# Kernel optimization log

Measured on AMD Instinct MI355X. Metric: run time of the kernel, lower is better.

The kernel has to match this reference:

```python
import jax, jax.numpy as jnp
import numpy as np

N, NS, C_IN, C_OUT = 20000, 32, 64, 128
V = (0.1, 0.1, 0.2)
BN_EPS = 1e-5


def setup_inputs() -> dict:
    key = jax.random.key(0)
    ks = jax.random.split(key, 5)
    features = jax.random.normal(ks[0], (N, NS, C_IN), jnp.float32)
    coords = jax.random.normal(ks[1], (N, NS, 3), jnp.float32)
    centers = jax.random.normal(ks[2], (N, 4), jnp.float32)
    mask = jax.random.randint(ks[3], (N, NS), 0, 2, jnp.int32)
    # Linear(C_IN, C_OUT, bias=False) weight, torch layout [out, in]
    W = jax.random.normal(ks[4], (C_OUT, C_IN), jnp.float32) / np.sqrt(C_IN)
    gamma = jnp.ones((C_OUT,), jnp.float32)   # BatchNorm1d weight
    beta = jnp.zeros((C_OUT,), jnp.float32)   # BatchNorm1d bias
    return dict(features=features, coords=coords, centers=centers, mask=mask,
                W=W, gamma=gamma, beta=beta)


def reference(features, coords, centers, mask, W, gamma, beta):
    # --- geometric features (no_grad in original) ---
    normalizer = jnp.array([V[0], V[1], V[2], V[0]**2 + V[1]**2 + V[2]**2],
                           dtype=jnp.float32)
    rel = coords - centers[:, 1:4][:, None, :]            # [N, NS, 3]
    dist = jnp.sum(rel * rel, axis=2, keepdims=True)       # [N, NS, 1]
    geo = jnp.concatenate([rel, dist], axis=2) / normalizer  # [N, NS, 4]

    # --- shared MLP: Linear -> BatchNorm1d (training stats) -> ReLU ---
    x = jnp.einsum('nsc,dc->nsd', features, W)             # [N, NS, C_OUT]
    xf = x.reshape(-1, C_OUT)
    mu = jnp.mean(xf, axis=0)
    var = jnp.mean((xf - mu) ** 2, axis=0)                 # biased var (torch BN)
    x = (x - mu) * jax.lax.rsqrt(var + BN_EPS) * gamma + beta
    x = jax.nn.relu(x)                                     # [N, NS, C_OUT]

    # --- weighted, masked mean pool over neighbors ---
    geo_rep = jnp.tile(geo, (1, 1, C_OUT // 4))            # [N, NS, C_OUT]
    m = mask.astype(jnp.float32)                           # [N, NS]
    num = jnp.sum(x * geo_rep * m[:, :, None], axis=1)     # [N, C_OUT]
    den = jnp.maximum(jnp.sum(m, axis=1, keepdims=True), 1.0)
    return num / den
```

## Files before the change

### kernel.cpp

```cpp
#include <hip/hip_runtime.h>
#include <hip/hip_bf16.h>

#define N_PTS 20000
#define NSAMP 32
#define CIN 64
#define COUT 128
#define M_ROWS (N_PTS * NSAMP)
#define TILES (M_ROWS / 64)
#define K1_BLOCKS 1024
#define K1_WAVES (K1_BLOCKS * 4)
#define BN_EPS 1e-5f

typedef __attribute__((ext_vector_type(8))) short short8v;
typedef __attribute__((ext_vector_type(4))) float f32x4;

__device__ inline short bf16_of(float f) {
    unsigned u = __float_as_uint(f);
    u = (u + 0x7FFFu + ((u >> 16) & 1u)) >> 16;
    return (short)u;
}

__global__ __launch_bounds__(256) void k1_stats(const float* __restrict__ F,
                                                float* __restrict__ Sp,
                                                float* __restrict__ Cp) {
    const int tid = threadIdx.x;
    const int wid = tid >> 6;
    const int lane = tid & 63;
    const int g = lane >> 4;
    const int i = lane & 15;
    const int gw = blockIdx.x * 4 + wid;

    f32x4 acc[4][4];
#pragma unroll
    for (int a = 0; a < 4; ++a)
#pragma unroll
        for (int b = 0; b < 4; ++b)
            acc[a][b] = (f32x4){0.f, 0.f, 0.f, 0.f};
    float colp[4] = {0.f, 0.f, 0.f, 0.f};

    for (int tile = gw; tile < TILES; tile += K1_WAVES) {
        const float* fb0 = F + (size_t)tile * 4096 + g * 512 + i;
        const float* fb1 = fb0 + 2048;
        short8v frag[4][2];
#pragma unroll
        for (int jt = 0; jt < 4; ++jt) {
            float cs = 0.f;
#pragma unroll
            for (int kk = 0; kk < 2; ++kk) {
                const float* p = kk ? fb1 : fb0;
                short8v fr;
#pragma unroll
                for (int r = 0; r < 8; ++r) {
                    float v = p[r * 64 + jt * 16];
                    cs += v;
                    fr[r] = bf16_of(v);
                }
                frag[jt][kk] = fr;
            }
            colp[jt] += cs;
        }
#pragma unroll
        for (int it = 0; it < 4; ++it)
#pragma unroll
            for (int jt = 0; jt < 4; ++jt) {
                acc[it][jt] = __builtin_amdgcn_mfma_f32_16x16x32_bf16(
                    frag[it][0], frag[jt][0], acc[it][jt], 0, 0, 0);
                acc[it][jt] = __builtin_amdgcn_mfma_f32_16x16x32_bf16(
                    frag[it][1], frag[jt][1], acc[it][jt], 0, 0, 0);
            }
    }

#pragma unroll
    for (int jt = 0; jt < 4; ++jt) {
        colp[jt] += __shfl_xor(colp[jt], 16);
        colp[jt] += __shfl_xor(colp[jt], 32);
    }
    if (lane < 16) {
#pragma unroll
        for (int jt = 0; jt < 4; ++jt)
            Cp[gw * 64 + jt * 16 + lane] = colp[jt];
    }

    __shared__ float sS[4096];
    for (int w = 0; w < 4; ++w) {
        if (wid == w) {
#pragma unroll
            for (int it = 0; it < 4; ++it)
#pragma unroll
                for (int jt = 0; jt < 4; ++jt)
#pragma unroll
                    for (int r = 0; r < 4; ++r) {
                        int idx = (it * 16 + g * 4 + r) * 64 + jt * 16 + i;
                        if (w == 0) sS[idx] = acc[it][jt][r];
                        else        sS[idx] += acc[it][jt][r];
                    }
        }
        __syncthreads();
    }
    float4* dst = (float4*)(Sp + (size_t)blockIdx.x * 4096);
    const float4* src = (const float4*)sS;
#pragma unroll
    for (int q = 0; q < 4; ++q)
        dst[q * 256 + tid] = src[q * 256 + tid];
}

__global__ __launch_bounds__(256) void kRedA(const float* __restrict__ Sp,
                                             const float* __restrict__ Cp,
                                             float* __restrict__ Tp,
                                             float* __restrict__ Tcp) {
    int t = blockIdx.x * 256 + threadIdx.x;
    if (t < 65536) {
        int o = t & 4095;
        int c = t >> 12;
        float s = 0.f;
#pragma unroll 8
        for (int b = 0; b < 64; ++b)
            s += Sp[(size_t)(c * 64 + b) * 4096 + o];
        Tp[t] = s;
    } else if (t < 65536 + 4096) {
        int u = t - 65536;
        int col = u & 63;
        int c = u >> 6;
        float s = 0.f;
#pragma unroll 8
        for (int w = 0; w < 64; ++w)
            s += Cp[(c * 64 + w) * 64 + col];
        Tcp[u] = s;
    }
}

__global__ __launch_bounds__(256) void kB(const float* __restrict__ Tp,
                                          const float* __restrict__ Tcp,
                                          const float* __restrict__ W,
                                          const float* __restrict__ gamma,
                                          const float* __restrict__ beta,
                                          float* __restrict__ scale,
                                          float* __restrict__ shift) {
    const int d = blockIdx.x;
    const int tid = threadIdx.x;
    __shared__ float sS[64 * 65];
    __shared__ float sw[64];

    for (int o = tid; o < 4096; o += 256) {
        float s = 0.f;
#pragma unroll
        for (int c = 0; c < 16; ++c) s += Tp[c * 4096 + o];
        sS[(o >> 6) * 65 + (o & 63)] = s;
    }
    if (tid < 64) sw[tid] = W[d * 64 + tid];
    __syncthreads();

    if (tid < 64) {
        float w_t = sw[tid];
        float rowdot = 0.f;
#pragma unroll
        for (int j = 0; j < 64; ++j) rowdot += sS[tid * 65 + j] * sw[j];
        float cs = 0.f;
#pragma unroll
        for (int c = 0; c < 64; ++c) cs += Tcp[c * 64 + tid];
        float p = w_t * rowdot;
        float mup = w_t * cs;
        for (int k = 1; k <= 32; k <<= 1) {
            p += __shfl_xor(p, k);
            mup += __shfl_xor(mup, k);
        }
        if (tid == 0) {
            const float invM = 1.f / (float)M_ROWS;
            float mu = mup * invM;
            float ex2 = p * invM;
            float var = ex2 - mu * mu;
            float rs = rsqrtf(var + BN_EPS);
            float sc = gamma[d] * rs;
            scale[d] = sc;
            shift[d] = beta[d] - mu * sc;
        }
    }
}

__global__ __launch_bounds__(256) void k2_main(const float* __restrict__ F,
                                               const float* __restrict__ coords,
                                               const float* __restrict__ centers,
                                               const int* __restrict__ mask,
                                               const float* __restrict__ W,
                                               const float* __restrict__ scale,
                                               const float* __restrict__ shift,
                                               float* __restrict__ out) {
    const int tid = threadIdx.x;
    const int wid = tid >> 6;
    const int lane = tid & 63;
    const int g = lane >> 4;
    const int i = lane & 15;
    const int n_base = (blockIdx.x * 4 + wid) * 4;

    float4 raw[8];
#define LOADA(nn)                                                            \
    do {                                                                     \
        const float* fb_ = F + ((size_t)(nn)*NSAMP) * 64;                    \
        _Pragma("unroll") for (int mt_ = 0; mt_ < 2; ++mt_)                  \
            _Pragma("unroll") for (int kk_ = 0; kk_ < 2; ++kk_) {            \
            const float* fp_ = fb_ + (mt_ * 16 + i) * 64 + kk_ * 32 + g * 8; \
            raw[mt_ * 4 + kk_ * 2 + 0] = *(const float4*)(fp_);              \
            raw[mt_ * 4 + kk_ * 2 + 1] = *(const float4*)(fp_ + 4);          \
        }                                                                    \
    } while (0)

    LOADA(n_base);

    short8v b[8][2];
#pragma unroll
    for (int t = 0; t < 8; ++t)
#pragma unroll
        for (int kk = 0; kk < 2; ++kk) {
            const float* wp = W + (t * 16 + i) * 64 + kk * 32 + g * 8;
            short8v fr;
#pragma unroll
            for (int r = 0; r < 8; ++r) fr[r] = bf16_of(wp[r]);
            b[t][kk] = fr;
        }
    float sc[8], sh[8];
#pragma unroll
    for (int t = 0; t < 8; ++t) {
        sc[t] = scale[t * 16 + i];
        sh[t] = shift[t * 16 + i];
    }

    __shared__ float geoM[4][32][4];
    const f32x4 Z = {0.f, 0.f, 0.f, 0.f};

    for (int it = 0; it < 4; ++it) {
        const int n = n_base + it;

        short8v a[2][2];
#pragma unroll
        for (int mt = 0; mt < 2; ++mt)
#pragma unroll
            for (int kk = 0; kk < 2; ++kk) {
                float4 lo = raw[mt * 4 + kk * 2 + 0];
                float4 hi = raw[mt * 4 + kk * 2 + 1];
                short8v fr;
                fr[0] = bf16_of(lo.x); fr[1] = bf16_of(lo.y);
                fr[2] = bf16_of(lo.z); fr[3] = bf16_of(lo.w);
                fr[4] = bf16_of(hi.x); fr[5] = bf16_of(hi.y);
                fr[6] = bf16_of(hi.z); fr[7] = bf16_of(hi.w);
                a[mt][kk] = fr;
            }

        if (it < 3) LOADA(n + 1);

        float m = 0.f;
        if (lane < 32) {
            const int s = lane;
            const float* cp = coords + ((size_t)n * NSAMP + s) * 3;
            float r0 = cp[0] - centers[n * 4 + 1];
            float r1 = cp[1] - centers[n * 4 + 2];
            float r2 = cp[2] - centers[n * 4 + 3];
            float dist = r0 * r0 + r1 * r1 + r2 * r2;
            m = (float)mask[n * NSAMP + s];
            float4 gm = make_float4(r0 * 10.f * m, r1 * 10.f * m,
                                    r2 * 5.f * m, dist * (1.f / 0.06f) * m);
            *(float4*)&geoM[wid][s][0] = gm;
        }
        float den = m;
        for (int k = 1; k <= 32; k <<= 1) den += __shfl_xor(den, k);
        float inv_den = 1.f / fmaxf(den, 1.f);

        __builtin_amdgcn_sched_barrier(0x7F);

        float gv[2][4];
        const int j0 = i & 3;
#pragma unroll
        for (int mt = 0; mt < 2; ++mt)
#pragma unroll
            for (int r = 0; r < 4; ++r)
                gv[mt][r] = geoM[wid][mt * 16 + g * 4 + r][j0];

#pragma unroll
        for (int t = 0; t < 8; ++t) {
            float nump = 0.f;
#pragma unroll
            for (int mt = 0; mt < 2; ++mt) {
                f32x4 acc = __builtin_amdgcn_mfma_f32_16x16x32_bf16(
                    a[mt][0], b[t][0], Z, 0, 0, 0);
                acc = __builtin_amdgcn_mfma_f32_16x16x32_bf16(
                    a[mt][1], b[t][1], acc, 0, 0, 0);
#pragma unroll
                for (int r = 0; r < 4; ++r) {
                    float v = fmaf(acc[r], sc[t], sh[t]);
                    v = fmaxf(v, 0.f);
                    nump = fmaf(v, gv[mt][r], nump);
                }
            }
            nump += __shfl_xor(nump, 16);
            nump += __shfl_xor(nump, 32);
            if (lane < 16)
                out[(size_t)n * COUT + t * 16 + lane] = nump * inv_den;
        }
    }
#undef LOADA
}

extern "C" void kernel_launch(void* const* d_in, const int* in_sizes, int n_in,
                              void* d_out, int out_size, void* d_ws, size_t ws_size,
                              hipStream_t stream) {
    const float* F = (const float*)d_in[0];
    const float* coords = (const float*)d_in[1];
    const float* centers = (const float*)d_in[2];
    const int* mask = (const int*)d_in[3];
    const float* W = (const float*)d_in[4];
    const float* gamma = (const float*)d_in[5];
    const float* beta = (const float*)d_in[6];
    float* out = (float*)d_out;

    float* wsf = (float*)d_ws;
    float* scale = wsf;
    float* shift = wsf + 128;
    float* Tp = wsf + 256;
    float* Tcp = Tp + 65536;
    float* Sp = Tcp + 4096;
    float* Cp = Sp + (size_t)K1_BLOCKS * 4096;

    k1_stats<<<K1_BLOCKS, 256, 0, stream>>>(F, Sp, Cp);
    kRedA<<<272, 256, 0, stream>>>(Sp, Cp, Tp, Tcp);
    kB<<<COUT, 256, 0, stream>>>(Tp, Tcp, W, gamma, beta, scale, shift);
    k2_main<<<1250, 256, 0, stream>>>(F, coords, centers, mask, W, scale, shift, out);
}
```

Measured before the change: 105.0 us.

## Use 1250 stats blocks with matching reduction chunks; drop manual prefetch in main kernel

```diff
diff --git a/kernel.cpp b/kernel.cpp
--- a/kernel.cpp
+++ b/kernel.cpp
@@ -7,8 +7,12 @@
 #define COUT 128
 #define M_ROWS (N_PTS * NSAMP)
 #define TILES (M_ROWS / 64)
-#define K1_BLOCKS 1024
+#define K1_BLOCKS 1250
 #define K1_WAVES (K1_BLOCKS * 4)
+#define SP_CHUNKS 25
+#define SP_DEPTH 50
+#define CP_CHUNKS 50
+#define CP_DEPTH 100
 #define BN_EPS 1e-5f
 
 typedef __attribute__((ext_vector_type(8))) short short8v;
@@ -109,22 +113,22 @@
                                              float* __restrict__ Tp,
                                              float* __restrict__ Tcp) {
     int t = blockIdx.x * 256 + threadIdx.x;
-    if (t < 65536) {
+    if (t < SP_CHUNKS * 4096) {
         int o = t & 4095;
         int c = t >> 12;
         float s = 0.f;
-#pragma unroll 8
-        for (int b = 0; b < 64; ++b)
-            s += Sp[(size_t)(c * 64 + b) * 4096 + o];
+#pragma unroll 10
+        for (int b = 0; b < SP_DEPTH; ++b)
+            s += Sp[(size_t)(c * SP_DEPTH + b) * 4096 + o];
         Tp[t] = s;
-    } else if (t < 65536 + 4096) {
-        int u = t - 65536;
+    } else if (t < SP_CHUNKS * 4096 + CP_CHUNKS * 64) {
+        int u = t - SP_CHUNKS * 4096;
         int col = u & 63;
         int c = u >> 6;
         float s = 0.f;
-#pragma unroll 8
-        for (int w = 0; w < 64; ++w)
-            s += Cp[(c * 64 + w) * 64 + col];
+#pragma unroll 10
+        for (int w = 0; w < CP_DEPTH; ++w)
+            s += Cp[(c * CP_DEPTH + w) * 64 + col];
         Tcp[u] = s;
     }
 }
@@ -144,7 +148,7 @@
     for (int o = tid; o < 4096; o += 256) {
         float s = 0.f;
 #pragma unroll
-        for (int c = 0; c < 16; ++c) s += Tp[c * 4096 + o];
+        for (int c = 0; c < SP_CHUNKS; ++c) s += Tp[c * 4096 + o];
         sS[(o >> 6) * 65 + (o & 63)] = s;
     }
     if (tid < 64) sw[tid] = W[d * 64 + tid];
@@ -157,7 +161,7 @@
         for (int j = 0; j < 64; ++j) rowdot += sS[tid * 65 + j] * sw[j];
         float cs = 0.f;
 #pragma unroll
-        for (int c = 0; c < 64; ++c) cs += Tcp[c * 64 + tid];
+        for (int c = 0; c < CP_CHUNKS; ++c) cs += Tcp[c * 64 + tid];
         float p = w_t * rowdot;
         float mup = w_t * cs;
         for (int k = 1; k <= 32; k <<= 1) {
@@ -192,20 +196,6 @@
     const int i = lane & 15;
     const int n_base = (blockIdx.x * 4 + wid) * 4;
 
-    float4 raw[8];
-#define LOADA(nn)                                                            \
-    do {                                                                     \
-        const float* fb_ = F + ((size_t)(nn)*NSAMP) * 64;                    \
-        _Pragma("unroll") for (int mt_ = 0; mt_ < 2; ++mt_)                  \
-            _Pragma("unroll") for (int kk_ = 0; kk_ < 2; ++kk_) {            \
-            const float* fp_ = fb_ + (mt_ * 16 + i) * 64 + kk_ * 32 + g * 8; \
-            raw[mt_ * 4 + kk_ * 2 + 0] = *(const float4*)(fp_);              \
-            raw[mt_ * 4 + kk_ * 2 + 1] = *(const float4*)(fp_ + 4);          \
-        }                                                                    \
-    } while (0)
-
-    LOADA(n_base);
-
     short8v b[8][2];
 #pragma unroll
     for (int t = 0; t < 8; ++t)
@@ -235,17 +225,13 @@
         for (int mt = 0; mt < 2; ++mt)
 #pragma unroll
             for (int kk = 0; kk < 2; ++kk) {
-                float4 lo = raw[mt * 4 + kk * 2 + 0];
-                float4 hi = raw[mt * 4 + kk * 2 + 1];
+                const float* fp =
+                    F + ((size_t)n * NSAMP + mt * 16 + i) * 64 + kk * 32 + g * 8;
                 short8v fr;
-                fr[0] = bf16_of(lo.x); fr[1] = bf16_of(lo.y);
-                fr[2] = bf16_of(lo.z); fr[3] = bf16_of(lo.w);
-                fr[4] = bf16_of(hi.x); fr[5] = bf16_of(hi.y);
-                fr[6] = bf16_of(hi.z); fr[7] = bf16_of(hi.w);
+#pragma unroll
+                for (int r = 0; r < 8; ++r) fr[r] = bf16_of(fp[r]);
                 a[mt][kk] = fr;
             }
-
-        if (it < 3) LOADA(n + 1);
 
         float m = 0.f;
         if (lane < 32) {
@@ -296,7 +282,6 @@
                 out[(size_t)n * COUT + t * 16 + lane] = nump * inv_den;
         }
     }
-#undef LOADA
 }
 
 extern "C" void kernel_launch(void* const* d_in, const int* in_sizes, int n_in,
@@ -315,12 +300,12 @@
     float* scale = wsf;
     float* shift = wsf + 128;
     float* Tp = wsf + 256;
-    float* Tcp = Tp + 65536;
-    float* Sp = Tcp + 4096;
+    float* Tcp = Tp + SP_CHUNKS * 4096;
+    float* Sp = Tcp + CP_CHUNKS * 64;
     float* Cp = Sp + (size_t)K1_BLOCKS * 4096;
 
     k1_stats<<<K1_BLOCKS, 256, 0, stream>>>(F, Sp, Cp);
-    kRedA<<<272, 256, 0, stream>>>(Sp, Cp, Tp, Tcp);
+    kRedA<<<413, 256, 0, stream>>>(Sp, Cp, Tp, Tcp);
     kB<<<COUT, 256, 0, stream>>>(Tp, Tcp, W, gamma, beta, scale, shift);
     k2_main<<<1250, 256, 0, stream>>>(F, coords, centers, mask, W, scale, shift, out);
 }
```

Measured after the change: 102.8 us. -2.1%, faster.
